# Kernel tuning notes

Measured on AMD Instinct MI355X. Metric: run time of the kernel, lower is better.

The kernel has to match this reference:

```python
import jax, jax.numpy as jnp
import numpy as np

B, C_IN, C_OUT, N, K = 4, 64, 64, 100000, 6
EPS = 1e-5  # BatchNorm2d default eps


def setup_inputs() -> dict:
    key = jax.random.key(0)
    k1, k2, k3, k4 = jax.random.split(key, 4)
    x = jax.random.normal(k1, (B, C_IN, N), jnp.float32)
    neigh = jax.random.randint(k2, (B, N, K), 0, N, jnp.int32)
    # bias-free 1x2 conv weights (center feature + neighbor-sum symmetric operator)
    W0 = jax.random.normal(k3, (C_OUT, C_IN, 2), jnp.float32) * (1.0 / np.sqrt(C_IN * 2))
    W1 = jax.random.normal(k4, (C_OUT, C_OUT, 2), jnp.float32) * (1.0 / np.sqrt(C_OUT * 2))
    gamma = jnp.ones((C_OUT,), jnp.float32)
    beta = jnp.zeros((C_OUT,), jnp.float32)
    return {"x": x, "neigh": neigh, "W0": W0, "W1": W1, "gamma": gamma, "beta": beta}


def _mesh_conv_point(x, neigh, W):
    # x: [B, C, N], neigh: [B, N, K] -> gather neighbor features [B, C, N, K]
    nb = jax.vmap(lambda xb, ib: xb[:, ib])(x, neigh)
    # symmetric operator stack: center feature and sum over neighbors -> [B, C, N, 2]
    G = jnp.stack([x, nb.sum(axis=-1)], axis=-1)
    # 1x2 conv (bias=False) as einsum -> [B, O, N]
    return jnp.einsum('bcns,ocs->bon', G, W)


def _batchnorm(h, gamma, beta):
    # training-mode batch stats over (batch, vertex) per channel
    mean = h.mean(axis=(0, 2), keepdims=True)
    var = h.var(axis=(0, 2), keepdims=True)
    return (h - mean) * jax.lax.rsqrt(var + EPS) * gamma[None, :, None] + beta[None, :, None]


def reference(x, neigh, W0, W1, gamma, beta):
    h = _mesh_conv_point(x, neigh, W0)
    x1 = h  # residual branch
    h = _batchnorm(jax.nn.relu(h), gamma, beta)
    h = _mesh_conv_point(h, neigh, W1)
    h = h + x1
    return jax.nn.relu(h)
```

## Files before the change

kernel.cpp:

```cpp
#include <hip/hip_runtime.h>
#include <hip/hip_bf16.h>

#define BB   4
#define NN   100000
#define TOT  (BB * NN)
#define KK   6
#define EPSV 1e-5f

using bf16   = __hip_bfloat16;
using ushort = unsigned short;
using uint32 = unsigned int;
typedef __attribute__((ext_vector_type(8))) short  short8;
typedef __attribute__((ext_vector_type(4))) float  float4v;

union U4S8 { uint4 u; short8 s; };

__device__ __forceinline__ unsigned f2bu(float f) {
    union { bf16 h; ushort u; } c; c.h = __float2bfloat16(f); return c.u;
}
__device__ __forceinline__ unsigned pk(float a, float b) {
    return f2bu(a) | (f2bu(b) << 16);
}
__device__ __forceinline__ float blo(unsigned x) {
    union { unsigned u; float f; } c; c.u = x << 16; return c.f;
}
__device__ __forceinline__ float bhi(unsigned x) {
    union { unsigned u; float f; } c; c.u = x & 0xFFFF0000u; return c.f;
}
__device__ __forceinline__ unsigned relu2(unsigned x) {
    unsigned lo = (unsigned)(((int)(x << 16)) >> 31) & 0x0000FFFFu;
    unsigned hi = ((unsigned)(((int)x) >> 31)) << 16;
    return x & ~(lo | hi);
}
__device__ __forceinline__ int batch_base(int g) {
    return (g >= 3 * NN) ? 3 * NN : (g >= 2 * NN) ? 2 * NN : (g >= NN) ? NN : 0;
}

#define ACC8(v)  { h[0]+=blo(v.x); h[1]+=bhi(v.x); h[2]+=blo(v.y); h[3]+=bhi(v.y); \
                   h[4]+=blo(v.z); h[5]+=bhi(v.z); h[6]+=blo(v.w); h[7]+=bhi(v.w); }
#define ACCR8(v) { unsigned a0=relu2(v.x),a1=relu2(v.y),a2=relu2(v.z),a3=relu2(v.w); \
                   h[0]+=blo(a0); h[1]+=bhi(a0); h[2]+=blo(a1); h[3]+=bhi(a1); \
                   h[4]+=blo(a2); h[5]+=bhi(a2); h[6]+=blo(a3); h[7]+=bhi(a3); }

__global__ void wprep0_k(const float* __restrict__ W0, ushort* __restrict__ Wf0)
{
    int L = blockIdx.x * 256 + threadIdx.x;
    if (L < 8192) {
        int i = L & 7, lane = (L >> 3) & 63, r = L >> 9;
        int t = r >> 2, ks = r & 3;
        int o = t * 16 + (lane & 15);
        int c = ks * 32 + (lane >> 4) * 8 + i;
        Wf0[L] = f2bu(W0[o * 128 + (c & 63) * 2 + (c >> 6)]);
    }
}

__global__ __launch_bounds__(256) void xpose_k(const float* __restrict__ x,
                                               ushort* __restrict__ xT)
{
    __shared__ uint32 tileP[64][36];
    const int b  = blockIdx.y;
    const int n0 = blockIdx.x * 64;
    const int tx = threadIdx.x & 63;
    const int ty = threadIdx.x >> 6;
    const float* xb = x + (size_t)b * 64 * NN;
    const int n = n0 + tx;
    const bool valid = (n < NN);
#pragma unroll
    for (int cc = 0; cc < 64; cc += 8) {
        const int c = cc + ty * 2;
        float a0 = valid ? xb[(size_t)c * NN + n] : 0.f;
        float a1 = valid ? xb[(size_t)(c + 1) * NN + n] : 0.f;
        tileP[tx][c >> 1] = pk(a0, a1);
    }
    __syncthreads();
    const int s  = threadIdx.x & 7;
    const int p0 = threadIdx.x >> 3;
#pragma unroll
    for (int t = 0; t < 2; ++t) {
        const int p  = p0 + t * 32;
        const int n2 = n0 + p;
        if (n2 < NN) {
            uint4 v = *(const uint4*)(&tileP[p][s * 4]);
            *(uint4*)(xT + ((size_t)b * NN + n2) * 64 + s * 8) = v;
        }
    }
}

__global__ __launch_bounds__(256, 4) void gatherx_k(
    const ushort* __restrict__ xT, const int* __restrict__ neigh,
    ushort* __restrict__ SX)
{
    const int wave = threadIdx.x >> 6;
    const int lane = threadIdx.x & 63;
    const int p    = lane >> 3;
    const int s    = lane & 7;
    const int so   = s * 8;
    const int g0   = (blockIdx.x * 4 + wave) * 32;

#pragma unroll
    for (int t = 0; t < 4; ++t) {
        const int gme = g0 + t * 8 + p;
        const int bo  = batch_base(gme);
        const int* np = neigh + (size_t)gme * 6;
        const uint2 i01 = *(const uint2*)(np);
        const uint2 i23 = *(const uint2*)(np + 2);
        const uint2 i45 = *(const uint2*)(np + 4);

        uint4 v0 = *(const uint4*)(xT + (size_t)(bo + (int)i01.x) * 64 + so);
        uint4 v1 = *(const uint4*)(xT + (size_t)(bo + (int)i01.y) * 64 + so);
        uint4 v2 = *(const uint4*)(xT + (size_t)(bo + (int)i23.x) * 64 + so);
        uint4 v3 = *(const uint4*)(xT + (size_t)(bo + (int)i23.y) * 64 + so);
        uint4 v4 = *(const uint4*)(xT + (size_t)(bo + (int)i45.x) * 64 + so);
        uint4 v5 = *(const uint4*)(xT + (size_t)(bo + (int)i45.y) * 64 + so);

        float h[8] = {0, 0, 0, 0, 0, 0, 0, 0};
        ACC8(v0) ACC8(v1) ACC8(v2) ACC8(v3) ACC8(v4) ACC8(v5)

        uint4 st;
        st.x = pk(h[0], h[1]); st.y = pk(h[2], h[3]);
        st.z = pk(h[4], h[5]); st.w = pk(h[6], h[7]);
        *(uint4*)(SX + (size_t)gme * 64 + so) = st;
    }
}

__global__ __launch_bounds__(256, 3) void gemm1_k(
    const ushort* __restrict__ xT, const ushort* __restrict__ SX,
    const ushort* __restrict__ Wf, ushort* __restrict__ hT,
    float* __restrict__ stats)
{
    __shared__ float red[4][128];
    const int wave = threadIdx.x >> 6;
    const int lane = threadIdx.x & 63;
    const int col  = lane & 15;
    const int quad = lane >> 4;

    short8 wf[4][4];
#pragma unroll
    for (int t = 0; t < 4; ++t)
#pragma unroll
        for (int ks = 0; ks < 4; ++ks)
            wf[t][ks] = *(const short8*)(Wf + ((t * 4 + ks) * 64 + lane) * 8);

    float sA[16], sB[16];
#pragma unroll
    for (int j = 0; j < 16; ++j) { sA[j] = 0.f; sB[j] = 0.f; }

    const int wid = blockIdx.x * 4 + wave;
    for (int tile = wid; tile < 25000; tile += 2500) {
        const size_t g0 = (size_t)tile * 16;
        const ushort* xr = xT + (g0 + col) * 64 + quad * 8;
        const ushort* sr = SX + (g0 + col) * 64 + quad * 8;
        short8 p0 = *(const short8*)(xr);
        short8 p1 = *(const short8*)(xr + 32);
        short8 p2 = *(const short8*)(sr);
        short8 p3 = *(const short8*)(sr + 32);

        float4v acc[4];
#pragma unroll
        for (int t = 0; t < 4; ++t) acc[t] = (float4v){0.f, 0.f, 0.f, 0.f};
#pragma unroll
        for (int t = 0; t < 4; ++t)
            acc[t] = __builtin_amdgcn_mfma_f32_16x16x32_bf16(wf[t][0], p0, acc[t], 0, 0, 0);
#pragma unroll
        for (int t = 0; t < 4; ++t)
            acc[t] = __builtin_amdgcn_mfma_f32_16x16x32_bf16(wf[t][1], p1, acc[t], 0, 0, 0);
#pragma unroll
        for (int t = 0; t < 4; ++t)
            acc[t] = __builtin_amdgcn_mfma_f32_16x16x32_bf16(wf[t][2], p2, acc[t], 0, 0, 0);
#pragma unroll
        for (int t = 0; t < 4; ++t)
            acc[t] = __builtin_amdgcn_mfma_f32_16x16x32_bf16(wf[t][3], p3, acc[t], 0, 0, 0);

#pragma unroll
        for (int t = 0; t < 4; ++t) {
            uint2 d;
            d.x = pk(acc[t][0], acc[t][1]);
            d.y = pk(acc[t][2], acc[t][3]);
            *(uint2*)(hT + (g0 + col) * 64 + t * 16 + quad * 4) = d;
#pragma unroll
            for (int r = 0; r < 4; ++r) {
                float rv = fmaxf(acc[t][r], 0.f);
                sA[t * 4 + r] += rv;
                sB[t * 4 + r]  = fmaf(rv, rv, sB[t * 4 + r]);
            }
        }
    }

#pragma unroll
    for (int d = 1; d < 16; d <<= 1)
#pragma unroll
        for (int j = 0; j < 16; ++j) {
            sA[j] += __shfl_xor(sA[j], d);
            sB[j] += __shfl_xor(sB[j], d);
        }
    if (col == 0) {
#pragma unroll
        for (int t = 0; t < 4; ++t)
#pragma unroll
            for (int r = 0; r < 4; ++r) {
                const int o = t * 16 + quad * 4 + r;
                red[wave][o]      = sA[t * 4 + r];
                red[wave][64 + o] = sB[t * 4 + r];
            }
    }
    __syncthreads();
    if (threadIdx.x < 128) {
        float v = red[0][threadIdx.x] + red[1][threadIdx.x]
                + red[2][threadIdx.x] + red[3][threadIdx.x];
        atomicAdd(&stats[threadIdx.x], v);
    }
}

__global__ void bnA_k(const float* __restrict__ stats, const float* __restrict__ gamma,
                      const float* __restrict__ beta, float* __restrict__ ab)
{
    const int o = threadIdx.x;
    if (o < 64) {
        const float inv = 1.f / (float)TOT;
        float mean = stats[o] * inv;
        float var  = stats[64 + o] * inv - mean * mean;
        float a    = gamma[o] * rsqrtf(var + EPSV);
        ab[o]      = a;
        ab[64 + o] = fmaf(-a, mean, beta[o]);
    }
}

__global__ __launch_bounds__(256) void bnB_k(
    const float* __restrict__ ab, const float* __restrict__ W1,
    ushort* __restrict__ Wf1, float* __restrict__ bias)
{
    if (blockIdx.x < 32) {
        int L = blockIdx.x * 256 + threadIdx.x;
        int i = L & 7, lane = (L >> 3) & 63, r = L >> 9;
        int t = r >> 2, ks = r & 3;
        int o = t * 16 + (lane & 15);
        int c = ks * 32 + (lane >> 4) * 8 + i;
        int cc = c & 63;
        Wf1[L] = f2bu(ab[cc] * W1[o * 128 + cc * 2 + (c >> 6)]);
    } else if (threadIdx.x < 64) {
        const int o = threadIdx.x;
        float s = 0.f;
#pragma unroll
        for (int c = 0; c < 64; ++c)
            s += ab[64 + c] * (W1[o * 128 + c * 2] + 6.f * W1[o * 128 + c * 2 + 1]);
        bias[o] = s;
    }
}

__global__ __launch_bounds__(256, 4) void gatherh_k(
    const ushort* __restrict__ hT, const int* __restrict__ neigh,
    ushort* __restrict__ SH)
{
    const int wave = threadIdx.x >> 6;
    const int lane = threadIdx.x & 63;
    const int p    = lane >> 3;
    const int s    = lane & 7;
    const int so   = s * 8;
    const int g0   = (blockIdx.x * 4 + wave) * 32;

#pragma unroll
    for (int t = 0; t < 4; ++t) {
        const int gme = g0 + t * 8 + p;
        const int bo  = batch_base(gme);
        const int* np = neigh + (size_t)gme * 6;
        const uint2 i01 = *(const uint2*)(np);
        const uint2 i23 = *(const uint2*)(np + 2);
        const uint2 i45 = *(const uint2*)(np + 4);

        uint4 v0 = *(const uint4*)(hT + (size_t)(bo + (int)i01.x) * 64 + so);
        uint4 v1 = *(const uint4*)(hT + (size_t)(bo + (int)i01.y) * 64 + so);
        uint4 v2 = *(const uint4*)(hT + (size_t)(bo + (int)i23.x) * 64 + so);
        uint4 v3 = *(const uint4*)(hT + (size_t)(bo + (int)i23.y) * 64 + so);
        uint4 v4 = *(const uint4*)(hT + (size_t)(bo + (int)i45.x) * 64 + so);
        uint4 v5 = *(const uint4*)(hT + (size_t)(bo + (int)i45.y) * 64 + so);

        float h[8] = {0, 0, 0, 0, 0, 0, 0, 0};
        ACCR8(v0) ACCR8(v1) ACCR8(v2) ACCR8(v3) ACCR8(v4) ACCR8(v5)

        uint4 st;
        st.x = pk(h[0], h[1]); st.y = pk(h[2], h[3]);
        st.z = pk(h[4], h[5]); st.w = pk(h[6], h[7]);
        *(uint4*)(SH + (size_t)gme * 64 + so) = st;
    }
}

__global__ __launch_bounds__(256, 3) void gemm2_k(
    const ushort* __restrict__ hT, const ushort* __restrict__ SH,
    const ushort* __restrict__ Wf, const float* __restrict__ bias,
    float* __restrict__ out)
{
    __shared__ float ts[64][65];
    const int wave = threadIdx.x >> 6;
    const int lane = threadIdx.x & 63;
    const int col  = lane & 15;
    const int quad = lane >> 4;

    short8 wf[4][4];
#pragma unroll
    for (int t = 0; t < 4; ++t)
#pragma unroll
        for (int ks = 0; ks < 4; ++ks)
            wf[t][ks] = *(const short8*)(Wf + ((t * 4 + ks) * 64 + lane) * 8);

    float binit[16];
#pragma unroll
    for (int t = 0; t < 4; ++t)
#pragma unroll
        for (int r = 0; r < 4; ++r)
            binit[t * 4 + r] = bias[t * 16 + quad * 4 + r];

    for (int it = 0; it < 10; ++it) {
        const int gb = (blockIdx.x * 10 + it) * 64;
        const size_t g0 = (size_t)gb + wave * 16;
        const ushort* hr = hT + (g0 + col) * 64 + quad * 8;
        const ushort* sr = SH + (g0 + col) * 64 + quad * 8;
        U4S8 p0, p1, p2, p3;
        p0.u = *(const uint4*)(hr);
        p1.u = *(const uint4*)(hr + 32);
        p2.u = *(const uint4*)(sr);
        p3.u = *(const uint4*)(sr + 32);
        p0.u.x = relu2(p0.u.x); p0.u.y = relu2(p0.u.y);
        p0.u.z = relu2(p0.u.z); p0.u.w = relu2(p0.u.w);
        p1.u.x = relu2(p1.u.x); p1.u.y = relu2(p1.u.y);
        p1.u.z = relu2(p1.u.z); p1.u.w = relu2(p1.u.w);

        float4v acc[4];
#pragma unroll
        for (int t = 0; t < 4; ++t)
            acc[t] = (float4v){binit[t * 4], binit[t * 4 + 1],
                               binit[t * 4 + 2], binit[t * 4 + 3]};
#pragma unroll
        for (int t = 0; t < 4; ++t)
            acc[t] = __builtin_amdgcn_mfma_f32_16x16x32_bf16(wf[t][0], p0.s, acc[t], 0, 0, 0);
#pragma unroll
        for (int t = 0; t < 4; ++t)
            acc[t] = __builtin_amdgcn_mfma_f32_16x16x32_bf16(wf[t][1], p1.s, acc[t], 0, 0, 0);
#pragma unroll
        for (int t = 0; t < 4; ++t)
            acc[t] = __builtin_amdgcn_mfma_f32_16x16x32_bf16(wf[t][2], p2.s, acc[t], 0, 0, 0);
#pragma unroll
        for (int t = 0; t < 4; ++t)
            acc[t] = __builtin_amdgcn_mfma_f32_16x16x32_bf16(wf[t][3], p3.s, acc[t], 0, 0, 0);

        const int pl = wave * 16 + col;
#pragma unroll
        for (int t = 0; t < 4; ++t) {
            const uint2 rd = *(const uint2*)(hT + (g0 + col) * 64 + t * 16 + quad * 4);
            const int o = t * 16 + quad * 4;
            ts[o + 0][pl] = fmaxf(acc[t][0] + blo(rd.x), 0.f);
            ts[o + 1][pl] = fmaxf(acc[t][1] + bhi(rd.x), 0.f);
            ts[o + 2][pl] = fmaxf(acc[t][2] + blo(rd.y), 0.f);
            ts[o + 3][pl] = fmaxf(acc[t][3] + bhi(rd.y), 0.f);
        }
        __syncthreads();

        const int g2  = gb + lane;
        const int bo2 = batch_base(g2);
        const int b2  = (g2 >= 3 * NN) ? 3 : (g2 >= 2 * NN) ? 2 : (g2 >= NN) ? 1 : 0;
        const int n2  = g2 - bo2;
#pragma unroll
        for (int r = 0; r < 16; ++r) {
            const int o = wave * 16 + r;
            out[((size_t)b2 * 64 + o) * NN + n2] = ts[o][lane];
        }
        __syncthreads();
    }
}

extern "C" void kernel_launch(void* const* d_in, const int* in_sizes, int n_in,
                              void* d_out, int out_size, void* d_ws, size_t ws_size,
                              hipStream_t stream)
{
    const float* x     = (const float*)d_in[0];
    const int*   neigh = (const int*)d_in[1];
    const float* W0    = (const float*)d_in[2];
    const float* W1    = (const float*)d_in[3];
    const float* gamma = (const float*)d_in[4];
    const float* beta  = (const float*)d_in[5];
    float* out = (float*)d_out;

    char* ws = (char*)d_ws;
    ushort* xT    = (ushort*)(ws + 0);
    ushort* SX    = (ushort*)(ws + 51200000);
    ushort* SH    = SX;
    ushort* hT    = (ushort*)(ws + 102400000);
    float*  stats = (float*)(ws + 153600000);
    float*  ab    = (float*)(ws + 153600512);
    ushort* Wf0   = (ushort*)(ws + 153601024);
    ushort* Wf1   = (ushort*)(ws + 153617408);
    float*  bias  = (float*)(ws + 153633792);

    hipMemsetAsync(stats, 0, 512, stream);
    wprep0_k<<<dim3(32), dim3(256), 0, stream>>>(W0, Wf0);
    xpose_k<<<dim3((NN + 63) / 64, BB), dim3(256), 0, stream>>>(x, xT);
    gatherx_k<<<dim3(3125), dim3(256), 0, stream>>>(xT, neigh, SX);
    gemm1_k<<<dim3(625), dim3(256), 0, stream>>>(xT, SX, Wf0, hT, stats);
    bnA_k<<<dim3(1), dim3(64), 0, stream>>>(stats, gamma, beta, ab);
    bnB_k<<<dim3(33), dim3(256), 0, stream>>>(ab, W1, Wf1, bias);
    gatherh_k<<<dim3(3125), dim3(256), 0, stream>>>(hT, neigh, SH);
    gemm2_k<<<dim3(625), dim3(256), 0, stream>>>(hT, SH, Wf1, bias, out);
}
```

Measured before the change: 371.3 us.

## Fuse neighbor gather-sum into both MFMA GEMM kernels, drop SX/SH buffers

Removes the separate gatherx and gatherh kernels. Each GEMM kernel now loads its tile's neighbor indices, gathers the neighbor rows and sums them in registers into the B operand for the MFMA. This avoids writing and re-reading the 51 MB SX/SH intermediates and saves two launches. In exchange, each lane issues 12 scattered 16-byte loads per tile, and launch bounds drop to 2 waves/SIMD with the grid doubled, which may limit latency hiding for the gathers.

```diff
diff --git a/kernel.cpp b/kernel.cpp
--- a/kernel.cpp
+++ b/kernel.cpp
@@ -38,9 +38,9 @@
 
 #define ACC8(v)  { h[0]+=blo(v.x); h[1]+=bhi(v.x); h[2]+=blo(v.y); h[3]+=bhi(v.y); \
                    h[4]+=blo(v.z); h[5]+=bhi(v.z); h[6]+=blo(v.w); h[7]+=bhi(v.w); }
-#define ACCR8(v) { unsigned a0=relu2(v.x),a1=relu2(v.y),a2=relu2(v.z),a3=relu2(v.w); \
-                   h[0]+=blo(a0); h[1]+=bhi(a0); h[2]+=blo(a1); h[3]+=bhi(a1); \
-                   h[4]+=blo(a2); h[5]+=bhi(a2); h[6]+=blo(a3); h[7]+=bhi(a3); }
+#define ACCR8(v) { unsigned _q0=relu2(v.x),_q1=relu2(v.y),_q2=relu2(v.z),_q3=relu2(v.w); \
+                   h[0]+=blo(_q0); h[1]+=bhi(_q0); h[2]+=blo(_q1); h[3]+=bhi(_q1); \
+                   h[4]+=blo(_q2); h[5]+=bhi(_q2); h[6]+=blo(_q3); h[7]+=bhi(_q3); }
 
 __global__ void wprep0_k(const float* __restrict__ W0, ushort* __restrict__ Wf0)
 {
@@ -86,45 +86,8 @@
     }
 }
 
-__global__ __launch_bounds__(256, 4) void gatherx_k(
+__global__ __launch_bounds__(256, 2) void gemm1_k(
     const ushort* __restrict__ xT, const int* __restrict__ neigh,
-    ushort* __restrict__ SX)
-{
-    const int wave = threadIdx.x >> 6;
-    const int lane = threadIdx.x & 63;
-    const int p    = lane >> 3;
-    const int s    = lane & 7;
-    const int so   = s * 8;
-    const int g0   = (blockIdx.x * 4 + wave) * 32;
-
-#pragma unroll
-    for (int t = 0; t < 4; ++t) {
-        const int gme = g0 + t * 8 + p;
-        const int bo  = batch_base(gme);
-        const int* np = neigh + (size_t)gme * 6;
-        const uint2 i01 = *(const uint2*)(np);
-        const uint2 i23 = *(const uint2*)(np + 2);
-        const uint2 i45 = *(const uint2*)(np + 4);
-
-        uint4 v0 = *(const uint4*)(xT + (size_t)(bo + (int)i01.x) * 64 + so);
-        uint4 v1 = *(const uint4*)(xT + (size_t)(bo + (int)i01.y) * 64 + so);
-        uint4 v2 = *(const uint4*)(xT + (size_t)(bo + (int)i23.x) * 64 + so);
-        uint4 v3 = *(const uint4*)(xT + (size_t)(bo + (int)i23.y) * 64 + so);
-        uint4 v4 = *(const uint4*)(xT + (size_t)(bo + (int)i45.x) * 64 + so);
-        uint4 v5 = *(const uint4*)(xT + (size_t)(bo + (int)i45.y) * 64 + so);
-
-        float h[8] = {0, 0, 0, 0, 0, 0, 0, 0};
-        ACC8(v0) ACC8(v1) ACC8(v2) ACC8(v3) ACC8(v4) ACC8(v5)
-
-        uint4 st;
-        st.x = pk(h[0], h[1]); st.y = pk(h[2], h[3]);
-        st.z = pk(h[4], h[5]); st.w = pk(h[6], h[7]);
-        *(uint4*)(SX + (size_t)gme * 64 + so) = st;
-    }
-}
-
-__global__ __launch_bounds__(256, 3) void gemm1_k(
-    const ushort* __restrict__ xT, const ushort* __restrict__ SX,
     const ushort* __restrict__ Wf, ushort* __restrict__ hT,
     float* __restrict__ stats)
 {
@@ -133,6 +96,7 @@
     const int lane = threadIdx.x & 63;
     const int col  = lane & 15;
     const int quad = lane >> 4;
+    const int co   = quad * 8;
 
     short8 wf[4][4];
 #pragma unroll
@@ -146,37 +110,69 @@
     for (int j = 0; j < 16; ++j) { sA[j] = 0.f; sB[j] = 0.f; }
 
     const int wid = blockIdx.x * 4 + wave;
-    for (int tile = wid; tile < 25000; tile += 2500) {
+    for (int i5 = 0; i5 < 5; ++i5) {
+        const int tile = wid * 5 + i5;
         const size_t g0 = (size_t)tile * 16;
-        const ushort* xr = xT + (g0 + col) * 64 + quad * 8;
-        const ushort* sr = SX + (g0 + col) * 64 + quad * 8;
-        short8 p0 = *(const short8*)(xr);
-        short8 p1 = *(const short8*)(xr + 32);
-        short8 p2 = *(const short8*)(sr);
-        short8 p3 = *(const short8*)(sr + 32);
+        const int gme  = (int)g0 + col;
+        const int bo   = batch_base(gme);
+        const int* np  = neigh + (size_t)gme * 6;
+        const uint2 i01 = *(const uint2*)(np);
+        const uint2 i23 = *(const uint2*)(np + 2);
+        const uint2 i45 = *(const uint2*)(np + 4);
+        const ushort* xb0 = xT + (size_t)bo * 64;
+
+        const ushort* xr = xT + (size_t)gme * 64 + co;
+        U4S8 c0, c1;
+        c0.u = *(const uint4*)(xr);
+        c1.u = *(const uint4*)(xr + 32);
+
+        uint4 ga0 = *(const uint4*)(xb0 + (size_t)(int)i01.x * 64 + co);
+        uint4 ga1 = *(const uint4*)(xb0 + (size_t)(int)i01.y * 64 + co);
+        uint4 ga2 = *(const uint4*)(xb0 + (size_t)(int)i23.x * 64 + co);
+        uint4 ga3 = *(const uint4*)(xb0 + (size_t)(int)i23.y * 64 + co);
+        uint4 ga4 = *(const uint4*)(xb0 + (size_t)(int)i45.x * 64 + co);
+        uint4 ga5 = *(const uint4*)(xb0 + (size_t)(int)i45.y * 64 + co);
+        uint4 gb0 = *(const uint4*)(xb0 + (size_t)(int)i01.x * 64 + 32 + co);
+        uint4 gb1 = *(const uint4*)(xb0 + (size_t)(int)i01.y * 64 + 32 + co);
+        uint4 gb2 = *(const uint4*)(xb0 + (size_t)(int)i23.x * 64 + 32 + co);
+        uint4 gb3 = *(const uint4*)(xb0 + (size_t)(int)i23.y * 64 + 32 + co);
+        uint4 gb4 = *(const uint4*)(xb0 + (size_t)(int)i45.x * 64 + 32 + co);
+        uint4 gb5 = *(const uint4*)(xb0 + (size_t)(int)i45.y * 64 + 32 + co);
+
+        float h[8] = {0, 0, 0, 0, 0, 0, 0, 0};
+        ACC8(ga0) ACC8(ga1) ACC8(ga2) ACC8(ga3) ACC8(ga4) ACC8(ga5)
+        U4S8 p2;
+        p2.u.x = pk(h[0], h[1]); p2.u.y = pk(h[2], h[3]);
+        p2.u.z = pk(h[4], h[5]); p2.u.w = pk(h[6], h[7]);
+#pragma unroll
+        for (int j = 0; j < 8; ++j) h[j] = 0.f;
+        ACC8(gb0) ACC8(gb1) ACC8(gb2) ACC8(gb3) ACC8(gb4) ACC8(gb5)
+        U4S8 p3;
+        p3.u.x = pk(h[0], h[1]); p3.u.y = pk(h[2], h[3]);
+        p3.u.z = pk(h[4], h[5]); p3.u.w = pk(h[6], h[7]);
 
         float4v acc[4];
 #pragma unroll
         for (int t = 0; t < 4; ++t) acc[t] = (float4v){0.f, 0.f, 0.f, 0.f};
 #pragma unroll
         for (int t = 0; t < 4; ++t)
-            acc[t] = __builtin_amdgcn_mfma_f32_16x16x32_bf16(wf[t][0], p0, acc[t], 0, 0, 0);
-#pragma unroll
-        for (int t = 0; t < 4; ++t)
-            acc[t] = __builtin_amdgcn_mfma_f32_16x16x32_bf16(wf[t][1], p1, acc[t], 0, 0, 0);
-#pragma unroll
-        for (int t = 0; t < 4; ++t)
-            acc[t] = __builtin_amdgcn_mfma_f32_16x16x32_bf16(wf[t][2], p2, acc[t], 0, 0, 0);
-#pragma unroll
-        for (int t = 0; t < 4; ++t)
-            acc[t] = __builtin_amdgcn_mfma_f32_16x16x32_bf16(wf[t][3], p3, acc[t], 0, 0, 0);
+            acc[t] = __builtin_amdgcn_mfma_f32_16x16x32_bf16(wf[t][0], c0.s, acc[t], 0, 0, 0);
+#pragma unroll
+        for (int t = 0; t < 4; ++t)
+            acc[t] = __builtin_amdgcn_mfma_f32_16x16x32_bf16(wf[t][1], c1.s, acc[t], 0, 0, 0);
+#pragma unroll
+        for (int t = 0; t < 4; ++t)
+            acc[t] = __builtin_amdgcn_mfma_f32_16x16x32_bf16(wf[t][2], p2.s, acc[t], 0, 0, 0);
+#pragma unroll
+        for (int t = 0; t < 4; ++t)
+            acc[t] = __builtin_amdgcn_mfma_f32_16x16x32_bf16(wf[t][3], p3.s, acc[t], 0, 0, 0);
 
 #pragma unroll
         for (int t = 0; t < 4; ++t) {
             uint2 d;
             d.x = pk(acc[t][0], acc[t][1]);
             d.y = pk(acc[t][2], acc[t][3]);
-            *(uint2*)(hT + (g0 + col) * 64 + t * 16 + quad * 4) = d;
+            *(uint2*)(hT + (size_t)gme * 64 + t * 16 + quad * 4) = d;
 #pragma unroll
             for (int r = 0; r < 4; ++r) {
                 float rv = fmaxf(acc[t][r], 0.f);
@@ -247,82 +243,75 @@
     }
 }
 
-__global__ __launch_bounds__(256, 4) void gatherh_k(
+__global__ __launch_bounds__(256, 2) void gemm2_k(
     const ushort* __restrict__ hT, const int* __restrict__ neigh,
-    ushort* __restrict__ SH)
-{
+    const ushort* __restrict__ Wf, const float* __restrict__ bias,
+    float* __restrict__ out)
+{
+    __shared__ float ts[64][65];
     const int wave = threadIdx.x >> 6;
     const int lane = threadIdx.x & 63;
-    const int p    = lane >> 3;
-    const int s    = lane & 7;
-    const int so   = s * 8;
-    const int g0   = (blockIdx.x * 4 + wave) * 32;
-
-#pragma unroll
-    for (int t = 0; t < 4; ++t) {
-        const int gme = g0 + t * 8 + p;
+    const int col  = lane & 15;
+    const int quad = lane >> 4;
+    const int co   = quad * 8;
+
+    short8 wf[4][4];
+#pragma unroll
+    for (int t = 0; t < 4; ++t)
+#pragma unroll
+        for (int ks = 0; ks < 4; ++ks)
+            wf[t][ks] = *(const short8*)(Wf + ((t * 4 + ks) * 64 + lane) * 8);
+
+    float binit[16];
+#pragma unroll
+    for (int t = 0; t < 4; ++t)
+#pragma unroll
+        for (int r = 0; r < 4; ++r)
+            binit[t * 4 + r] = bias[t * 16 + quad * 4 + r];
+
+    for (int it = 0; it < 5; ++it) {
+        const int gb = (blockIdx.x * 5 + it) * 64;
+        const int gme = gb + wave * 16 + col;
         const int bo  = batch_base(gme);
         const int* np = neigh + (size_t)gme * 6;
         const uint2 i01 = *(const uint2*)(np);
         const uint2 i23 = *(const uint2*)(np + 2);
         const uint2 i45 = *(const uint2*)(np + 4);
-
-        uint4 v0 = *(const uint4*)(hT + (size_t)(bo + (int)i01.x) * 64 + so);
-        uint4 v1 = *(const uint4*)(hT + (size_t)(bo + (int)i01.y) * 64 + so);
-        uint4 v2 = *(const uint4*)(hT + (size_t)(bo + (int)i23.x) * 64 + so);
-        uint4 v3 = *(const uint4*)(hT + (size_t)(bo + (int)i23.y) * 64 + so);
-        uint4 v4 = *(const uint4*)(hT + (size_t)(bo + (int)i45.x) * 64 + so);
-        uint4 v5 = *(const uint4*)(hT + (size_t)(bo + (int)i45.y) * 64 + so);
+        const ushort* hb0 = hT + (size_t)bo * 64;
+
+        const ushort* hr = hT + (size_t)gme * 64 + co;
+        U4S8 c0, c1;
+        c0.u = *(const uint4*)(hr);
+        c1.u = *(const uint4*)(hr + 32);
+        c0.u.x = relu2(c0.u.x); c0.u.y = relu2(c0.u.y);
+        c0.u.z = relu2(c0.u.z); c0.u.w = relu2(c0.u.w);
+        c1.u.x = relu2(c1.u.x); c1.u.y = relu2(c1.u.y);
+        c1.u.z = relu2(c1.u.z); c1.u.w = relu2(c1.u.w);
+
+        uint4 ga0 = *(const uint4*)(hb0 + (size_t)(int)i01.x * 64 + co);
+        uint4 ga1 = *(const uint4*)(hb0 + (size_t)(int)i01.y * 64 + co);
+        uint4 ga2 = *(const uint4*)(hb0 + (size_t)(int)i23.x * 64 + co);
+        uint4 ga3 = *(const uint4*)(hb0 + (size_t)(int)i23.y * 64 + co);
+        uint4 ga4 = *(const uint4*)(hb0 + (size_t)(int)i45.x * 64 + co);
+        uint4 ga5 = *(const uint4*)(hb0 + (size_t)(int)i45.y * 64 + co);
+        uint4 gb0 = *(const uint4*)(hb0 + (size_t)(int)i01.x * 64 + 32 + co);
+        uint4 gb1 = *(const uint4*)(hb0 + (size_t)(int)i01.y * 64 + 32 + co);
+        uint4 gb2 = *(const uint4*)(hb0 + (size_t)(int)i23.x * 64 + 32 + co);
+        uint4 gb3 = *(const uint4*)(hb0 + (size_t)(int)i23.y * 64 + 32 + co);
+        uint4 gb4 = *(const uint4*)(hb0 + (size_t)(int)i45.x * 64 + 32 + co);
+        uint4 gb5 = *(const uint4*)(hb0 + (size_t)(int)i45.y * 64 + 32 + co);
 
         float h[8] = {0, 0, 0, 0, 0, 0, 0, 0};
-        ACCR8(v0) ACCR8(v1) ACCR8(v2) ACCR8(v3) ACCR8(v4) ACCR8(v5)
-
-        uint4 st;
-        st.x = pk(h[0], h[1]); st.y = pk(h[2], h[3]);
-        st.z = pk(h[4], h[5]); st.w = pk(h[6], h[7]);
-        *(uint4*)(SH + (size_t)gme * 64 + so) = st;
-    }
-}
-
-__global__ __launch_bounds__(256, 3) void gemm2_k(
-    const ushort* __restrict__ hT, const ushort* __restrict__ SH,
-    const ushort* __restrict__ Wf, const float* __restrict__ bias,
-    float* __restrict__ out)
-{
-    __shared__ float ts[64][65];
-    const int wave = threadIdx.x >> 6;
-    const int lane = threadIdx.x & 63;
-    const int col  = lane & 15;
-    const int quad = lane >> 4;
-
-    short8 wf[4][4];
-#pragma unroll
-    for (int t = 0; t < 4; ++t)
-#pragma unroll
-        for (int ks = 0; ks < 4; ++ks)
-            wf[t][ks] = *(const short8*)(Wf + ((t * 4 + ks) * 64 + lane) * 8);
-
-    float binit[16];
-#pragma unroll
-    for (int t = 0; t < 4; ++t)
-#pragma unroll
-        for (int r = 0; r < 4; ++r)
-            binit[t * 4 + r] = bias[t * 16 + quad * 4 + r];
-
-    for (int it = 0; it < 10; ++it) {
-        const int gb = (blockIdx.x * 10 + it) * 64;
-        const size_t g0 = (size_t)gb + wave * 16;
-        const ushort* hr = hT + (g0 + col) * 64 + quad * 8;
-        const ushort* sr = SH + (g0 + col) * 64 + quad * 8;
-        U4S8 p0, p1, p2, p3;
-        p0.u = *(const uint4*)(hr);
-        p1.u = *(const uint4*)(hr + 32);
-        p2.u = *(const uint4*)(sr);
-        p3.u = *(const uint4*)(sr + 32);
-        p0.u.x = relu2(p0.u.x); p0.u.y = relu2(p0.u.y);
-        p0.u.z = relu2(p0.u.z); p0.u.w = relu2(p0.u.w);
-        p1.u.x = relu2(p1.u.x); p1.u.y = relu2(p1.u.y);
-        p1.u.z = relu2(p1.u.z); p1.u.w = relu2(p1.u.w);
+        ACCR8(ga0) ACCR8(ga1) ACCR8(ga2) ACCR8(ga3) ACCR8(ga4) ACCR8(ga5)
+        U4S8 p2;
+        p2.u.x = pk(h[0], h[1]); p2.u.y = pk(h[2], h[3]);
+        p2.u.z = pk(h[4], h[5]); p2.u.w = pk(h[6], h[7]);
+#pragma unroll
+        for (int j = 0; j < 8; ++j) h[j] = 0.f;
+        ACCR8(gb0) ACCR8(gb1) ACCR8(gb2) ACCR8(gb3) ACCR8(gb4) ACCR8(gb5)
+        U4S8 p3;
+        p3.u.x = pk(h[0], h[1]); p3.u.y = pk(h[2], h[3]);
+        p3.u.z = pk(h[4], h[5]); p3.u.w = pk(h[6], h[7]);
 
         float4v acc[4];
 #pragma unroll
@@ -331,10 +320,10 @@
                                binit[t * 4 + 2], binit[t * 4 + 3]};
 #pragma unroll
         for (int t = 0; t < 4; ++t)
-            acc[t] = __builtin_amdgcn_mfma_f32_16x16x32_bf16(wf[t][0], p0.s, acc[t], 0, 0, 0);
-#pragma unroll
-        for (int t = 0; t < 4; ++t)
-            acc[t] = __builtin_amdgcn_mfma_f32_16x16x32_bf16(wf[t][1], p1.s, acc[t], 0, 0, 0);
+            acc[t] = __builtin_amdgcn_mfma_f32_16x16x32_bf16(wf[t][0], c0.s, acc[t], 0, 0, 0);
+#pragma unroll
+        for (int t = 0; t < 4; ++t)
+            acc[t] = __builtin_amdgcn_mfma_f32_16x16x32_bf16(wf[t][1], c1.s, acc[t], 0, 0, 0);
 #pragma unroll
         for (int t = 0; t < 4; ++t)
             acc[t] = __builtin_amdgcn_mfma_f32_16x16x32_bf16(wf[t][2], p2.s, acc[t], 0, 0, 0);
@@ -345,7 +334,7 @@
         const int pl = wave * 16 + col;
 #pragma unroll
         for (int t = 0; t < 4; ++t) {
-            const uint2 rd = *(const uint2*)(hT + (g0 + col) * 64 + t * 16 + quad * 4);
+            const uint2 rd = *(const uint2*)(hT + (size_t)gme * 64 + t * 16 + quad * 4);
             const int o = t * 16 + quad * 4;
             ts[o + 0][pl] = fmaxf(acc[t][0] + blo(rd.x), 0.f);
             ts[o + 1][pl] = fmaxf(acc[t][1] + bhi(rd.x), 0.f);
@@ -356,12 +345,12 @@
 
         const int g2  = gb + lane;
         const int bo2 = batch_base(g2);
-        const int b2  = (g2 >= 3 * NN) ? 3 : (g2 >= 2 * NN) ? 2 : (g2 >= NN) ? 1 : 0;
+        const int bb2 = (g2 >= 3 * NN) ? 3 : (g2 >= 2 * NN) ? 2 : (g2 >= NN) ? 1 : 0;
         const int n2  = g2 - bo2;
 #pragma unroll
         for (int r = 0; r < 16; ++r) {
             const int o = wave * 16 + r;
-            out[((size_t)b2 * 64 + o) * NN + n2] = ts[o][lane];
+            out[((size_t)bb2 * 64 + o) * NN + n2] = ts[o][lane];
         }
         __syncthreads();
     }
@@ -381,8 +370,6 @@
 
     char* ws = (char*)d_ws;
     ushort* xT    = (ushort*)(ws + 0);
-    ushort* SX    = (ushort*)(ws + 51200000);
-    ushort* SH    = SX;
     ushort* hT    = (ushort*)(ws + 102400000);
     float*  stats = (float*)(ws + 153600000);
     float*  ab    = (float*)(ws + 153600512);
@@ -393,10 +380,8 @@
     hipMemsetAsync(stats, 0, 512, stream);
     wprep0_k<<<dim3(32), dim3(256), 0, stream>>>(W0, Wf0);
     xpose_k<<<dim3((NN + 63) / 64, BB), dim3(256), 0, stream>>>(x, xT);
-    gatherx_k<<<dim3(3125), dim3(256), 0, stream>>>(xT, neigh, SX);
-    gemm1_k<<<dim3(625), dim3(256), 0, stream>>>(xT, SX, Wf0, hT, stats);
+    gemm1_k<<<dim3(1250), dim3(256), 0, stream>>>(xT, neigh, Wf0, hT, stats);
     bnA_k<<<dim3(1), dim3(64), 0, stream>>>(stats, gamma, beta, ab);
     bnB_k<<<dim3(33), dim3(256), 0, stream>>>(ab, W1, Wf1, bias);
-    gatherh_k<<<dim3(3125), dim3(256), 0, stream>>>(hT, neigh, SH);
-    gemm2_k<<<dim3(625), dim3(256), 0, stream>>>(hT, SH, Wf1, bias, out);
-}
+    gemm2_k<<<dim3(1250), dim3(256), 0, stream>>>(hT, neigh, Wf1, bias, out);
+}
```

Result: faster. 358.2 us (-3.5%).
